# Kernel tuning notes

Measured on AMD Instinct MI355X. Metric: run time of the kernel, lower is better.

Reference implementation:

```python
import jax, jax.numpy as jnp
import numpy as np

D_IN = 32
K = 16


def cbr(x, W, s, b):
    # 1x1 Conv2d + folded (eval-mode) BatchNorm + ReLU, channels-last.
    return jax.nn.relu(jnp.einsum('...i,io->...o', x, W) * s + b)


def gather_neighbour(pc, idx):
    # pc: [B, N, d]; idx: [B, N, K] -> [B, N, K, d]
    B, N, d = pc.shape
    g = jnp.take_along_axis(pc, idx.reshape(B, -1, 1), axis=1)
    return g.reshape(B, N, K, d)


def setup_inputs() -> dict:
    key = jax.random.key(0)
    ks = jax.random.split(key, 32)
    B, N = 2, 65536

    def w(k, ci, co):
        return jax.random.normal(k, (ci, co), jnp.float32) * (1.0 / np.sqrt(ci))

    inp = {
        'feature': jax.random.normal(ks[0], (B, D_IN, N, 1), jnp.float32),
        'xyz': jax.random.normal(ks[1], (B, N, 3), jnp.float32),
        'neigh_idx': jax.random.randint(ks[2], (B, N, K), 0, N, jnp.int64),
        # TNet
        'tW1': w(ks[3], 3, 16),  'ts1': jnp.ones(16),  'tb1': jnp.zeros(16),
        'tW2': w(ks[4], 16, 64), 'ts2': jnp.ones(64),  'tb2': jnp.zeros(64),
        'tW3': w(ks[5], 64, 16), 'ts3': jnp.ones(16),  'tb3': jnp.zeros(16),
        'tW4': w(ks[6], 16, 9),  'tb4': jnp.zeros(9),
        # RFA mlps
        'W1': w(ks[7], 3, 3),            's1': jnp.ones(3),     'b1': jnp.zeros(3),
        'W2': w(ks[8], D_IN, D_IN),      's2': jnp.ones(D_IN),  'b2': jnp.zeros(D_IN),
        'W3': w(ks[9], D_IN + 3, D_IN),  's3': jnp.ones(D_IN),  'b3': jnp.zeros(D_IN),
        'W4': w(ks[10], 2 * D_IN, D_IN), 's4': jnp.ones(D_IN),  'b4': jnp.zeros(D_IN),
    }
    return inp


def tnet(xyz, tW1, ts1, tb1, tW2, ts2, tb2, tW3, ts3, tb3, tW4, tb4):
    h = cbr(xyz, tW1, ts1, tb1)          # [B, N, 16]
    h = cbr(h, tW2, ts2, tb2)            # [B, N, 64]
    h = jnp.max(h, axis=1, keepdims=True)  # [B, 1, 64]
    h = cbr(h, tW3, ts3, tb3)            # [B, 1, 16]
    h = jnp.einsum('...i,io->...o', h, tW4) + tb4  # [B, 1, 9] (no bn/act)
    dia = jnp.eye(3, dtype=h.dtype).reshape(1, 1, 9)
    return (h + dia).reshape(-1, 3, 3)


def reference(feature, xyz, neigh_idx,
              tW1, ts1, tb1, tW2, ts2, tb2, tW3, ts3, tb3, tW4, tb4,
              W1, s1, b1, W2, s2, b2, W3, s3, b3, W4, s4, b4):
    # channels-last features [B, N, d_in]
    feat = feature.squeeze(-1).transpose(0, 2, 1)

    t = tnet(xyz, tW1, ts1, tb1, tW2, ts2, tb2, tW3, ts3, tb3, tW4, tb4)
    f_xyz = jnp.einsum('bni,bij->bnj', xyz, t)   # [B, N, 3]
    f_xyz = cbr(f_xyz, W1, s1, b1)               # [B, N, 3]
    f_xyz = gather_neighbour(f_xyz, neigh_idx)   # [B, N, K, 3]

    f_nei = cbr(feat, W2, s2, b2)                # [B, N, d]
    f_nei = gather_neighbour(f_nei, neigh_idx)   # [B, N, K, d]

    f_cat = jnp.concatenate([f_nei, f_xyz], axis=-1)  # [B, N, K, d+3]
    f_cat = cbr(f_cat, W3, s3, b3)               # [B, N, K, d]
    f_cat = jnp.max(f_cat, axis=2)               # max pooling over K -> [B, N, d]

    f = jnp.concatenate([feat, f_cat], axis=-1)  # [B, N, 2d]
    f = cbr(f, W4, s4, b4)                       # [B, N, d_in]
    return f.transpose(0, 2, 1)[..., None]       # [B, d_in, N, 1]
```

## Files before the change

kernel.cpp:

```cpp
#include <hip/hip_runtime.h>

#define NPTS   65536
#define TOTAL  (2 * NPTS)
#define NUNITS 1024

typedef __attribute__((ext_vector_type(8)))  short short8;
typedef __attribute__((ext_vector_type(16))) float float16;
union F8 { uint4 u; short8 s; };

#define WS_STRIPE 0
#define WS_T1A    8192
#define WS_T1B    (8192 + TOTAL * 64)
#define WS_T2     (8192 + TOTAL * 64 + TOTAL * 8)

__device__ __forceinline__ unsigned short f2bf(float x) {
    unsigned u = __float_as_uint(x);
    return (unsigned short)((u + 0x7FFFu + ((u >> 16) & 1u)) >> 16);
}
__device__ __forceinline__ unsigned pk2(float a, float b) {
    return (unsigned)f2bf(a) | ((unsigned)f2bf(b) << 16);
}
__device__ __forceinline__ float relu(float x) { return x > 0.f ? x : 0.f; }
__device__ __forceinline__ uint4 pk8(const float* e) {
    uint4 u;
    u.x = pk2(e[0], e[1]); u.y = pk2(e[2], e[3]);
    u.z = pk2(e[4], e[5]); u.w = pk2(e[6], e[7]);
    return u;
}
__device__ __forceinline__ float16 zero16() {
    float16 z;
#pragma unroll
    for (int i = 0; i < 16; i++) z[i] = 0.f;
    return z;
}

__global__ __launch_bounds__(256) void kP0(
    const float* __restrict__ feature, const float* __restrict__ xyz,
    const float* __restrict__ tW1, const float* __restrict__ ts1, const float* __restrict__ tb1,
    const float* __restrict__ tW2, const float* __restrict__ ts2, const float* __restrict__ tb2,
    const float* __restrict__ W2,  const float* __restrict__ s2,  const float* __restrict__ b2,
    char* ws)
{
    __shared__ float red[4][64];
    float* stripe       = (float*)(ws + WS_STRIPE);
    unsigned short* t1a = (unsigned short*)(ws + WS_T1A);
    unsigned short* t2  = (unsigned short*)(ws + WS_T2);
    const int lane = threadIdx.x & 63, wv = threadIdx.x >> 6;
    const int col = lane & 31, h = lane >> 5;
    const float16 z = zero16();
    const int u = blockIdx.x;
    const int b = u >> 9;
    float e[8];
    float aw0[8], aw1[8], aw2[8], bb[8];
#pragma unroll
    for (int j = 0; j < 8; j++) {
        int k = 8 * h + j; float s = ts1[k];
        aw0[j] = tW1[k] * s; aw1[j] = tW1[16 + k] * s; aw2[j] = tW1[32 + k] * s;
        bb[j] = tb1[k];
    }
    F8 bf0, bf1;
#pragma unroll
    for (int j = 0; j < 8; j++) e[j] = tW2[(8 * h + j) * 64 + col] * ts2[col];
    bf0.u = pk8(e);
#pragma unroll
    for (int j = 0; j < 8; j++) e[j] = tW2[(8 * h + j) * 64 + 32 + col] * ts2[32 + col];
    bf1.u = pk8(e);
    F8 a0, a1;
    float sc2 = s2[col];
#pragma unroll
    for (int j = 0; j < 8; j++) e[j] = W2[(8 * h + j) * 32 + col] * sc2;
    a0.u = pk8(e);
#pragma unroll
    for (int j = 0; j < 8; j++) e[j] = W2[(16 + 8 * h + j) * 32 + col] * sc2;
    a1.u = pk8(e);
    float b2v[16];
#pragma unroll
    for (int r = 0; r < 16; r++) b2v[r] = b2[(r & 3) + 8 * (r >> 2) + 4 * h];

    int base = u * 128 + wv * 32;
    const float* xp = xyz + (size_t)(base + col) * 3;
    float x0 = xp[0], x1 = xp[1], x2 = xp[2];
    float hv[8];
#pragma unroll
    for (int j = 0; j < 8; j++)
        hv[j] = relu(x0 * aw0[j] + x1 * aw1[j] + x2 * aw2[j] + bb[j]);
    F8 af; af.u = pk8(hv);
    float16 c0 = __builtin_amdgcn_mfma_f32_32x32x16_bf16(af.s, bf0.s, z, 0, 0, 0);
    float16 c1 = __builtin_amdgcn_mfma_f32_32x32x16_bf16(af.s, bf1.s, z, 0, 0, 0);
    float v0 = c0[0], v1 = c1[0];
#pragma unroll
    for (int i = 1; i < 16; i++) { v0 = fmaxf(v0, c0[i]); v1 = fmaxf(v1, c1[i]); }
    v0 = fmaxf(v0, __shfl_xor(v0, 32));
    v1 = fmaxf(v1, __shfl_xor(v1, 32));
    if (h == 0) { red[wv][col] = v0; red[wv][32 + col] = v1; }
    __syncthreads();
    if (threadIdx.x < 64) {
        int c = threadIdx.x;
        float m = fmaxf(fmaxf(red[0][c], red[1][c]), fmaxf(red[2][c], red[3][c]));
        float val = relu(m + tb2[c]);
        atomicMax((unsigned*)(stripe + (u & 15) * 128 + b * 64 + c), __float_as_uint(val));
    }
    int pt = base + col;
    const float* fb = feature + (size_t)b * 32 * NPTS + (pt & (NPTS - 1));
    float v[8];
    F8 f0, f1;
#pragma unroll
    for (int j = 0; j < 8; j++) v[j] = fb[(size_t)(8 * h + j) * NPTS];
    f0.u = pk8(v);
#pragma unroll
    for (int j = 0; j < 8; j++) v[j] = fb[(size_t)(16 + 8 * h + j) * NPTS];
    f1.u = pk8(v);
    *(uint4*)(t2 + (size_t)pt * 32 + 8 * h) = f0.u;
    *(uint4*)(t2 + (size_t)pt * 32 + 16 + 8 * h) = f1.u;
    float16 acc = z;
    acc = __builtin_amdgcn_mfma_f32_32x32x16_bf16(a0.s, f0.s, acc, 0, 0, 0);
    acc = __builtin_amdgcn_mfma_f32_32x32x16_bf16(a1.s, f1.s, acc, 0, 0, 0);
#pragma unroll
    for (int q = 0; q < 4; q++) {
        int r = 4 * q;
        uint2 uu;
        uu.x = pk2(relu(acc[r] + b2v[r]), relu(acc[r + 1] + b2v[r + 1]));
        uu.y = pk2(relu(acc[r + 2] + b2v[r + 2]), relu(acc[r + 3] + b2v[r + 3]));
        *(uint2*)(t1a + (size_t)pt * 32 + 8 * q + 4 * h) = uu;
    }
}

__global__ __launch_bounds__(256) void kP1(
    const float* __restrict__ xyz,
    const float* __restrict__ tW3, const float* __restrict__ ts3, const float* __restrict__ tb3,
    const float* __restrict__ tW4, const float* __restrict__ tb4,
    const float* __restrict__ W1,  const float* __restrict__ s1, const float* __restrict__ b1,
    char* ws)
{
    const float* stripe = (const float*)(ws + WS_STRIPE);
    unsigned short* t1b = (unsigned short*)(ws + WS_T1B);
    const int lane = threadIdx.x & 63, wv = threadIdx.x >> 6;
    const int col = lane & 31, h = lane >> 5;
    const int u = blockIdx.x;
    const int b = u >> 9;
    float hm = 0.f;
#pragma unroll
    for (int s = 0; s < 16; s++)
        hm = fmaxf(hm, stripe[s * 128 + b * 64 + lane]);
    float v[16];
    const float4* trow = (const float4*)(tW3 + lane * 16);
#pragma unroll
    for (int q = 0; q < 4; q++) {
        float4 t4 = trow[q];
        v[4 * q + 0] = hm * t4.x; v[4 * q + 1] = hm * t4.y;
        v[4 * q + 2] = hm * t4.z; v[4 * q + 3] = hm * t4.w;
    }
#pragma unroll
    for (int off = 1; off < 64; off <<= 1) {
#pragma unroll
        for (int c = 0; c < 16; c++) v[c] += __shfl_xor(v[c], off);
    }
    float T[9];
#pragma unroll
    for (int j = 0; j < 9; j++) T[j] = tb4[j];
#pragma unroll
    for (int c = 0; c < 16; c++) {
        float h3 = relu(v[c] * ts3[c] + tb3[c]);
#pragma unroll
        for (int j = 0; j < 9; j++) T[j] += h3 * tW4[c * 9 + j];
    }
    T[0] += 1.f; T[4] += 1.f; T[8] += 1.f;

    int pt = u * 128 + wv * 32 + col;
    const float* xp = xyz + (size_t)pt * 3;
    float x0 = xp[0], x1 = xp[1], x2 = xp[2];
    float q0 = x0 * T[0] + x1 * T[3] + x2 * T[6];
    float q1 = x0 * T[1] + x1 * T[4] + x2 * T[7];
    float q2 = x0 * T[2] + x1 * T[5] + x2 * T[8];
    float r0 = relu((q0 * W1[0] + q1 * W1[3] + q2 * W1[6]) * s1[0] + b1[0]);
    float r1 = relu((q0 * W1[1] + q1 * W1[4] + q2 * W1[7]) * s1[1] + b1[1]);
    float r2 = relu((q0 * W1[2] + q1 * W1[5] + q2 * W1[8]) * s1[2] + b1[2]);
    if (h == 0) {
        uint2 uu; uu.x = pk2(r0, r1); uu.y = pk2(r2, 0.f);
        *(uint2*)(t1b + (size_t)pt * 4) = uu;
    }
}

__global__ __launch_bounds__(256) void kP23(
    const int* __restrict__ nidx,
    const float* __restrict__ W3, const float* __restrict__ s3, const float* __restrict__ b3,
    const float* __restrict__ W4, const float* __restrict__ s4, const float* __restrict__ b4,
    char* ws, float* __restrict__ out)
{
    __shared__ unsigned short mld[128 * 36];
    const unsigned short* t1a = (const unsigned short*)(ws + WS_T1A);
    const unsigned short* t1b = (const unsigned short*)(ws + WS_T1B);
    const unsigned short* t2  = (const unsigned short*)(ws + WS_T2);
    const int lane = threadIdx.x & 63, wv = threadIdx.x >> 6;
    const int col = lane & 31, h = lane >> 5;
    const float16 z = zero16();
    float e[8];
    F8 w0, w1, w2, zf;
    zf.u.x = zf.u.y = zf.u.z = zf.u.w = 0u;
    float sc3 = s3[col];
#pragma unroll
    for (int j = 0; j < 8; j++) e[j] = W3[(8 * h + j) * 32 + col] * sc3;
    w0.u = pk8(e);
#pragma unroll
    for (int j = 0; j < 8; j++) e[j] = W3[(16 + 8 * h + j) * 32 + col] * sc3;
    w1.u = pk8(e);
    w2 = zf;
    if (h == 0) {
        float e2[8] = {0.f, 0.f, 0.f, 0.f, 0.f, 0.f, 0.f, 0.f};
#pragma unroll
        for (int j = 0; j < 3; j++) e2[j] = W3[(32 + j) * 32 + col] * sc3;
        w2.u = pk8(e2);
    }
    float b3v = b3[col];
    F8 aw[4];
    float sc4 = s4[col];
#pragma unroll
    for (int t = 0; t < 4; t++) {
#pragma unroll
        for (int j = 0; j < 8; j++) e[j] = W4[(16 * t + 8 * h + j) * 32 + col] * sc4;
        aw[t].u = pk8(e);
    }
    float b4v[16];
#pragma unroll
    for (int r = 0; r < 16; r++) b4v[r] = b4[(r & 3) + 8 * (r >> 2) + 4 * h];

    int slot = blockIdx.x & 7, batch = slot >> 2;
    int grp = (blockIdx.x >> 3) * 4 + (slot & 3);
    int u = batch * 512 + grp;
    int base = u * 128;

    int idxs[16];
#pragma unroll
    for (int it = 0; it < 16; it++)
        idxs[it] = nidx[(base + 2 * (wv * 16 + it)) * 16 + col];

    F8 na0, na1, na2;
    {
        size_t row = ((size_t)batch << 16) + (unsigned)idxs[0];
        const unsigned short* ap = t1a + row * 32;
        na0.u = *(const uint4*)(ap + 8 * h);
        na1.u = *(const uint4*)(ap + 16 + 8 * h);
        na2 = zf;
        if (h == 0) { uint2 q = *(const uint2*)(t1b + row * 4); na2.u.x = q.x; na2.u.y = q.y; }
    }
    for (int it = 0; it < 16; it++) {
        F8 ca0 = na0, ca1 = na1, ca2 = na2;
        if (it < 15) {
            size_t row = ((size_t)batch << 16) + (unsigned)idxs[it + 1];
            const unsigned short* ap = t1a + row * 32;
            na0.u = *(const uint4*)(ap + 8 * h);
            na1.u = *(const uint4*)(ap + 16 + 8 * h);
            na2 = zf;
            if (h == 0) { uint2 q = *(const uint2*)(t1b + row * 4); na2.u.x = q.x; na2.u.y = q.y; }
        }
        float16 acc = z;
        acc = __builtin_amdgcn_mfma_f32_32x32x16_bf16(ca0.s, w0.s, acc, 0, 0, 0);
        acc = __builtin_amdgcn_mfma_f32_32x32x16_bf16(ca1.s, w1.s, acc, 0, 0, 0);
        acc = __builtin_amdgcn_mfma_f32_32x32x16_bf16(ca2.s, w2.s, acc, 0, 0, 0);
        float vA = acc[0], vB = acc[8];
#pragma unroll
        for (int r = 1; r < 8; r++) { vA = fmaxf(vA, acc[r]); vB = fmaxf(vB, acc[8 + r]); }
        vA = fmaxf(vA, __shfl_xor(vA, 32));
        vB = fmaxf(vB, __shfl_xor(vB, 32));
        vA = relu(vA + b3v);
        vB = relu(vB + b3v);
        float val = h ? vB : vA;
        int pi = wv * 16 + it;
        mld[(2 * pi + h) * 36 + col] = f2bf(val);
    }

    int p_loc = wv * 32 + col;
    int p = base + p_loc;
    const unsigned short* bp = t2 + (size_t)p * 32 + 8 * h;
    F8 x0, x1, x2, x3;
    x0.u = *(const uint4*)(bp);
    x1.u = *(const uint4*)(bp + 16);
    const unsigned short* mp = mld + p_loc * 36;
    uint2 q0 = *(const uint2*)(mp + 8 * h);
    uint2 q1 = *(const uint2*)(mp + 8 * h + 4);
    uint2 q2 = *(const uint2*)(mp + 16 + 8 * h);
    uint2 q3 = *(const uint2*)(mp + 16 + 8 * h + 4);
    x2.u.x = q0.x; x2.u.y = q0.y; x2.u.z = q1.x; x2.u.w = q1.y;
    x3.u.x = q2.x; x3.u.y = q2.y; x3.u.z = q3.x; x3.u.w = q3.y;
    float16 acc = z;
    acc = __builtin_amdgcn_mfma_f32_32x32x16_bf16(aw[0].s, x0.s, acc, 0, 0, 0);
    acc = __builtin_amdgcn_mfma_f32_32x32x16_bf16(aw[1].s, x1.s, acc, 0, 0, 0);
    acc = __builtin_amdgcn_mfma_f32_32x32x16_bf16(aw[2].s, x2.s, acc, 0, 0, 0);
    acc = __builtin_amdgcn_mfma_f32_32x32x16_bf16(aw[3].s, x3.s, acc, 0, 0, 0);
    float* ob = out + (size_t)(batch * 32) * NPTS + (p & (NPTS - 1));
#pragma unroll
    for (int r = 0; r < 16; r++) {
        int o = (r & 3) + 8 * (r >> 2) + 4 * h;
        ob[(size_t)o * NPTS] = relu(acc[r] + b4v[r]);
    }
}

extern "C" void kernel_launch(void* const* d_in, const int* in_sizes, int n_in,
                              void* d_out, int out_size, void* d_ws, size_t ws_size,
                              hipStream_t stream)
{
    const float* feature = (const float*)d_in[0];
    const float* xyz     = (const float*)d_in[1];
    const int*   nidx    = (const int*)d_in[2];
    const float* tW1 = (const float*)d_in[3];
    const float* ts1 = (const float*)d_in[4];
    const float* tb1 = (const float*)d_in[5];
    const float* tW2 = (const float*)d_in[6];
    const float* ts2 = (const float*)d_in[7];
    const float* tb2 = (const float*)d_in[8];
    const float* tW3 = (const float*)d_in[9];
    const float* ts3 = (const float*)d_in[10];
    const float* tb3 = (const float*)d_in[11];
    const float* tW4 = (const float*)d_in[12];
    const float* tb4 = (const float*)d_in[13];
    const float* W1  = (const float*)d_in[14];
    const float* s1  = (const float*)d_in[15];
    const float* b1  = (const float*)d_in[16];
    const float* W2  = (const float*)d_in[17];
    const float* s2  = (const float*)d_in[18];
    const float* b2  = (const float*)d_in[19];
    const float* W3  = (const float*)d_in[20];
    const float* s3  = (const float*)d_in[21];
    const float* b3  = (const float*)d_in[22];
    const float* W4  = (const float*)d_in[23];
    const float* s4  = (const float*)d_in[24];
    const float* b4  = (const float*)d_in[25];
    (void)in_sizes; (void)n_in; (void)out_size; (void)ws_size;

    char* wsp = (char*)d_ws;
    float* outp = (float*)d_out;

    hipMemsetAsync(wsp + WS_STRIPE, 0, 16 * 128 * sizeof(float), stream);
    kP0<<<NUNITS, 256, 0, stream>>>(feature, xyz, tW1, ts1, tb1, tW2, ts2, tb2,
                                    W2, s2, b2, wsp);
    kP1<<<NUNITS, 256, 0, stream>>>(xyz, tW3, ts3, tb3, tW4, tb4, W1, s1, b1, wsp);
    kP23<<<NUNITS, 256, 0, stream>>>(nidx, W3, s3, b3, W4, s4, b4, wsp, outp);
}
```

Measured before the change: 163.9 us.

## Fuse TNet tail and xyz transform into gather kernel, dropping kP1

Removes the separate kP1 launch. Each kP23 block now recomputes the 3x3 TNet transform from the stripe maxima and applies the transform plus the W1 conv to gathered raw xyz on the fly, instead of gathering a precomputed bf16 t1b buffer. The per-thread neighbour indices are also packed two per register as 16-bit values to save registers. The cost is redundant per-block TNet-tail work, a 16x recomputation of the xyz MLP per neighbour, and three scalar xyz loads per gather in place of one 8-byte load.

```diff
diff --git a/kernel.cpp b/kernel.cpp
--- a/kernel.cpp
+++ b/kernel.cpp
@@ -125,75 +125,61 @@
     }
 }
 
-__global__ __launch_bounds__(256) void kP1(
-    const float* __restrict__ xyz,
+__global__ __launch_bounds__(256) void kP23(
+    const int* __restrict__ nidx, const float* __restrict__ xyz,
     const float* __restrict__ tW3, const float* __restrict__ ts3, const float* __restrict__ tb3,
     const float* __restrict__ tW4, const float* __restrict__ tb4,
-    const float* __restrict__ W1,  const float* __restrict__ s1, const float* __restrict__ b1,
-    char* ws)
-{
-    const float* stripe = (const float*)(ws + WS_STRIPE);
-    unsigned short* t1b = (unsigned short*)(ws + WS_T1B);
-    const int lane = threadIdx.x & 63, wv = threadIdx.x >> 6;
-    const int col = lane & 31, h = lane >> 5;
-    const int u = blockIdx.x;
-    const int b = u >> 9;
-    float hm = 0.f;
-#pragma unroll
-    for (int s = 0; s < 16; s++)
-        hm = fmaxf(hm, stripe[s * 128 + b * 64 + lane]);
-    float v[16];
-    const float4* trow = (const float4*)(tW3 + lane * 16);
-#pragma unroll
-    for (int q = 0; q < 4; q++) {
-        float4 t4 = trow[q];
-        v[4 * q + 0] = hm * t4.x; v[4 * q + 1] = hm * t4.y;
-        v[4 * q + 2] = hm * t4.z; v[4 * q + 3] = hm * t4.w;
-    }
-#pragma unroll
-    for (int off = 1; off < 64; off <<= 1) {
-#pragma unroll
-        for (int c = 0; c < 16; c++) v[c] += __shfl_xor(v[c], off);
-    }
-    float T[9];
-#pragma unroll
-    for (int j = 0; j < 9; j++) T[j] = tb4[j];
-#pragma unroll
-    for (int c = 0; c < 16; c++) {
-        float h3 = relu(v[c] * ts3[c] + tb3[c]);
-#pragma unroll
-        for (int j = 0; j < 9; j++) T[j] += h3 * tW4[c * 9 + j];
-    }
-    T[0] += 1.f; T[4] += 1.f; T[8] += 1.f;
-
-    int pt = u * 128 + wv * 32 + col;
-    const float* xp = xyz + (size_t)pt * 3;
-    float x0 = xp[0], x1 = xp[1], x2 = xp[2];
-    float q0 = x0 * T[0] + x1 * T[3] + x2 * T[6];
-    float q1 = x0 * T[1] + x1 * T[4] + x2 * T[7];
-    float q2 = x0 * T[2] + x1 * T[5] + x2 * T[8];
-    float r0 = relu((q0 * W1[0] + q1 * W1[3] + q2 * W1[6]) * s1[0] + b1[0]);
-    float r1 = relu((q0 * W1[1] + q1 * W1[4] + q2 * W1[7]) * s1[1] + b1[1]);
-    float r2 = relu((q0 * W1[2] + q1 * W1[5] + q2 * W1[8]) * s1[2] + b1[2]);
-    if (h == 0) {
-        uint2 uu; uu.x = pk2(r0, r1); uu.y = pk2(r2, 0.f);
-        *(uint2*)(t1b + (size_t)pt * 4) = uu;
-    }
-}
-
-__global__ __launch_bounds__(256) void kP23(
-    const int* __restrict__ nidx,
-    const float* __restrict__ W3, const float* __restrict__ s3, const float* __restrict__ b3,
-    const float* __restrict__ W4, const float* __restrict__ s4, const float* __restrict__ b4,
+    const float* __restrict__ W1,  const float* __restrict__ s1,  const float* __restrict__ b1,
+    const float* __restrict__ W3,  const float* __restrict__ s3,  const float* __restrict__ b3,
+    const float* __restrict__ W4,  const float* __restrict__ s4,  const float* __restrict__ b4,
     char* ws, float* __restrict__ out)
 {
     __shared__ unsigned short mld[128 * 36];
+    const float* stripe = (const float*)(ws + WS_STRIPE);
     const unsigned short* t1a = (const unsigned short*)(ws + WS_T1A);
-    const unsigned short* t1b = (const unsigned short*)(ws + WS_T1B);
     const unsigned short* t2  = (const unsigned short*)(ws + WS_T2);
     const int lane = threadIdx.x & 63, wv = threadIdx.x >> 6;
     const int col = lane & 31, h = lane >> 5;
     const float16 z = zero16();
+
+    int slot = blockIdx.x & 7, batch = slot >> 2;
+    int grp = (blockIdx.x >> 3) * 4 + (slot & 3);
+    int u = batch * 512 + grp;
+    int base = u * 128;
+
+    float hm = 0.f;
+#pragma unroll
+    for (int s = 0; s < 16; s++)
+        hm = fmaxf(hm, stripe[s * 128 + batch * 64 + lane]);
+    float vv[16];
+    {
+        const float4* trow = (const float4*)(tW3 + lane * 16);
+#pragma unroll
+        for (int q = 0; q < 4; q++) {
+            float4 t4 = trow[q];
+            vv[4 * q + 0] = hm * t4.x; vv[4 * q + 1] = hm * t4.y;
+            vv[4 * q + 2] = hm * t4.z; vv[4 * q + 3] = hm * t4.w;
+        }
+    }
+#pragma unroll
+    for (int off = 1; off < 64; off <<= 1) {
+#pragma unroll
+        for (int c = 0; c < 16; c++) vv[c] += __shfl_xor(vv[c], off);
+    }
+    float T[9];
+#pragma unroll
+    for (int j = 0; j < 9; j++) T[j] = tb4[j];
+#pragma unroll
+    for (int c = 0; c < 16; c++) {
+        float h3 = relu(vv[c] * ts3[c] + tb3[c]);
+#pragma unroll
+        for (int j = 0; j < 9; j++) T[j] += h3 * tW4[c * 9 + j];
+    }
+    T[0] += 1.f; T[4] += 1.f; T[8] += 1.f;
+#pragma unroll
+    for (int j = 0; j < 9; j++)
+        T[j] = __uint_as_float(__builtin_amdgcn_readfirstlane(__float_as_uint(T[j])));
+
     float e[8];
     F8 w0, w1, w2, zf;
     zf.u.x = zf.u.y = zf.u.z = zf.u.w = 0u;
@@ -224,34 +210,51 @@
 #pragma unroll
     for (int r = 0; r < 16; r++) b4v[r] = b4[(r & 3) + 8 * (r >> 2) + 4 * h];
 
-    int slot = blockIdx.x & 7, batch = slot >> 2;
-    int grp = (blockIdx.x >> 3) * 4 + (slot & 3);
-    int u = batch * 512 + grp;
-    int base = u * 128;
-
-    int idxs[16];
-#pragma unroll
-    for (int it = 0; it < 16; it++)
-        idxs[it] = nidx[(base + 2 * (wv * 16 + it)) * 16 + col];
-
-    F8 na0, na1, na2;
+    unsigned idxp[8];
+#pragma unroll
+    for (int i2 = 0; i2 < 8; i2++) {
+        unsigned lo = (unsigned)nidx[(base + 2 * (wv * 16 + 2 * i2)) * 16 + col];
+        unsigned hi = (unsigned)nidx[(base + 2 * (wv * 16 + 2 * i2 + 1)) * 16 + col];
+        idxp[i2] = (lo & 0xffffu) | (hi << 16);
+    }
+
+    F8 na0, na1;
+    float nx0 = 0.f, nx1 = 0.f, nx2 = 0.f;
     {
-        size_t row = ((size_t)batch << 16) + (unsigned)idxs[0];
-        const unsigned short* ap = t1a + row * 32;
+        unsigned row = idxp[0] & 0xffffu;
+        size_t g = ((size_t)batch << 16) + row;
+        const unsigned short* ap = t1a + g * 32;
         na0.u = *(const uint4*)(ap + 8 * h);
         na1.u = *(const uint4*)(ap + 16 + 8 * h);
-        na2 = zf;
-        if (h == 0) { uint2 q = *(const uint2*)(t1b + row * 4); na2.u.x = q.x; na2.u.y = q.y; }
-    }
+        if (h == 0) {
+            const float* xp = xyz + g * 3;
+            nx0 = xp[0]; nx1 = xp[1]; nx2 = xp[2];
+        }
+    }
+#pragma unroll
     for (int it = 0; it < 16; it++) {
-        F8 ca0 = na0, ca1 = na1, ca2 = na2;
+        F8 ca0 = na0, ca1 = na1;
+        float cx0 = nx0, cx1 = nx1, cx2 = nx2;
         if (it < 15) {
-            size_t row = ((size_t)batch << 16) + (unsigned)idxs[it + 1];
-            const unsigned short* ap = t1a + row * 32;
+            unsigned row = (idxp[(it + 1) >> 1] >> (16 * ((it + 1) & 1))) & 0xffffu;
+            size_t g = ((size_t)batch << 16) + row;
+            const unsigned short* ap = t1a + g * 32;
             na0.u = *(const uint4*)(ap + 8 * h);
             na1.u = *(const uint4*)(ap + 16 + 8 * h);
-            na2 = zf;
-            if (h == 0) { uint2 q = *(const uint2*)(t1b + row * 4); na2.u.x = q.x; na2.u.y = q.y; }
+            if (h == 0) {
+                const float* xp = xyz + g * 3;
+                nx0 = xp[0]; nx1 = xp[1]; nx2 = xp[2];
+            }
+        }
+        F8 ca2 = zf;
+        if (h == 0) {
+            float q0 = cx0 * T[0] + cx1 * T[3] + cx2 * T[6];
+            float q1 = cx0 * T[1] + cx1 * T[4] + cx2 * T[7];
+            float q2 = cx0 * T[2] + cx1 * T[5] + cx2 * T[8];
+            float r0 = relu((q0 * W1[0] + q1 * W1[3] + q2 * W1[6]) * s1[0] + b1[0]);
+            float r1 = relu((q0 * W1[1] + q1 * W1[4] + q2 * W1[7]) * s1[1] + b1[1]);
+            float r2 = relu((q0 * W1[2] + q1 * W1[5] + q2 * W1[8]) * s1[2] + b1[2]);
+            ca2.u.x = pk2(r0, r1); ca2.u.y = pk2(r2, 0.f);
         }
         float16 acc = z;
         acc = __builtin_amdgcn_mfma_f32_32x32x16_bf16(ca0.s, w0.s, acc, 0, 0, 0);
@@ -333,6 +336,6 @@
     hipMemsetAsync(wsp + WS_STRIPE, 0, 16 * 128 * sizeof(float), stream);
     kP0<<<NUNITS, 256, 0, stream>>>(feature, xyz, tW1, ts1, tb1, tW2, ts2, tb2,
                                     W2, s2, b2, wsp);
-    kP1<<<NUNITS, 256, 0, stream>>>(xyz, tW3, ts3, tb3, tW4, tb4, W1, s1, b1, wsp);
-    kP23<<<NUNITS, 256, 0, stream>>>(nidx, W3, s3, b3, W4, s4, b4, wsp, outp);
-}
+    kP23<<<NUNITS, 256, 0, stream>>>(nidx, xyz, tW3, ts3, tb3, tW4, tb4,
+                                     W1, s1, b1, W3, s3, b3, W4, s4, b4, wsp, outp);
+}
```

Result: no change. 163.7 us (-0.1%).
